# Kernel optimization log

Hardware: AMD Instinct MI355X
Metric: run time of the kernel (lower is better)

The kernel has to match this reference:

```python
import jax, jax.numpy as jnp
import numpy as np

NUM_USERS = 100000
NUM_ITEMS = 50000
N = NUM_USERS + NUM_ITEMS
E = 3000000
DIM = 64


def setup_inputs() -> dict:
    key = jax.random.key(0)
    ks = jax.random.split(key, 8)
    emb_users = 0.01 * jax.random.normal(ks[0], (NUM_USERS, DIM), dtype=jnp.float32)
    emb_items = 0.01 * jax.random.normal(ks[1], (NUM_ITEMS, DIM), dtype=jnp.float32)
    # GCNConv linear weights (bias separate, as in PyG: lin(bias=False) + bias param)
    s = 1.0 / np.sqrt(DIM)
    W1 = jax.random.uniform(ks[2], (DIM, DIM), jnp.float32, -s, s)
    b1 = jnp.zeros((DIM,), jnp.float32)
    W2 = jax.random.uniform(ks[3], (DIM, DIM), jnp.float32, -s, s)
    b2 = jnp.zeros((DIM,), jnp.float32)
    edge_index = jax.random.randint(ks[4], (2, E), 0, N, dtype=jnp.int64)
    edge_weight = jax.random.uniform(ks[5], (E,), jnp.float32)
    return {"emb_users": emb_users, "emb_items": emb_items,
            "W1": W1, "b1": b1, "W2": W2, "b2": b2,
            "edge_index": edge_index, "edge_weight": edge_weight}


def _gcn_conv(x, W, b, row, col):
    """PyG GCNConv with add_self_loops=True, improved=False, unit edge weights.
    out[i] = sum_{j->i} d_j^-1/2 d_i^-1/2 (x_j W) + d_i^-1 (x_i W) + b
    where d includes the self-loop (+1).
    """
    n = x.shape[0]
    xw = x @ W                                           # [N, D]
    deg = jax.ops.segment_sum(jnp.ones_like(row, dtype=x.dtype), col,
                              num_segments=n) + 1.0      # in-degree + self-loop
    dinv = jax.lax.rsqrt(deg)                            # [N]
    coef = dinv[row] * dinv[col]                         # [E]
    msg = xw[row] * coef[:, None]                        # gather + scale  [E, D]
    out = jax.ops.segment_sum(msg, col, num_segments=n)  # scatter-add     [N, D]
    out = out + xw * (dinv * dinv)[:, None]              # self-loop term
    return out + b


def reference(emb_users, emb_items, W1, b1, W2, b2, edge_index, edge_weight):
    # edge_weight is accepted by forward() but never passed to the GCN convs
    row, col = edge_index[0], edge_index[1]
    emb = jnp.concatenate([emb_users, emb_items], axis=0)  # [N, D]
    embs = [emb]
    for W, b in ((W1, b1), (W2, b2)):
        emb = _gcn_conv(emb, W, b, row, col)
        embs.append(emb)
        emb = jax.nn.relu(emb)
    return jnp.stack(embs)  # [num_layers+1, N, D]
```

## Files before the change

kernel.cpp:

```cpp
#include <hip/hip_runtime.h>
#include <hip/hip_fp16.h>

#define DIM 64
#define BPN 1024
#define ECHUNK 8192
#define MAXNB 160

typedef _Float16 f16x8 __attribute__((ext_vector_type(8)));
typedef float f32x4 __attribute__((ext_vector_type(4)));


__global__ __launch_bounds__(1024) void bucket_count_kernel(
    const int* __restrict__ col, int* __restrict__ bucket_cnt, int E, int NB) {
  __shared__ int h[MAXNB];
  for (int t = threadIdx.x; t < NB; t += blockDim.x) h[t] = 0;
  __syncthreads();
  int base = blockIdx.x * ECHUNK;
  int end = min(base + ECHUNK, E);
  for (int e = base + (int)threadIdx.x; e < end; e += blockDim.x)
    atomicAdd(&h[col[e] >> 10], 1);
  __syncthreads();
  for (int t = threadIdx.x; t < NB; t += blockDim.x)
    if (h[t]) atomicAdd(&bucket_cnt[t], h[t]);
}

__global__ void bucket_scan_kernel(const int* __restrict__ bucket_cnt,
                                   int* __restrict__ bucket_base,
                                   int* __restrict__ bucket_cursor,
                                   int* __restrict__ off, int NB, int N, int E) {
  if (threadIdx.x == 0) {
    int s = 0;
    for (int b = 0; b < NB; b++) { bucket_base[b] = s; bucket_cursor[b] = s; s += bucket_cnt[b]; }
    bucket_base[NB] = s;
    off[N] = E;
  }
}

__global__ __launch_bounds__(1024) void bucket_scatter_kernel(
    const int* __restrict__ row, const int* __restrict__ col,
    int* __restrict__ bucket_cursor, int* __restrict__ packed, int E, int NB) {
  __shared__ int h[MAXNB];
  __shared__ int excl0[MAXNB];
  __shared__ int cur[MAXNB];
  __shared__ int gbase[MAXNB];
  __shared__ int staging[ECHUNK];
  __shared__ unsigned short map[ECHUNK];
  const int tid = threadIdx.x;
  for (int t = tid; t < NB; t += blockDim.x) h[t] = 0;
  __syncthreads();
  int base = blockIdx.x * ECHUNK;
  int end = min(base + ECHUNK, E);
  int total = end - base;
  for (int e = base + tid; e < end; e += blockDim.x)
    atomicAdd(&h[col[e] >> 10], 1);
  __syncthreads();
  if (tid == 0) {
    int s = 0;
    for (int b = 0; b < NB; b++) { excl0[b] = s; cur[b] = s; s += h[b]; }
  }
  __syncthreads();
  if (tid < NB) {
    if (h[tid] > 0) gbase[tid] = atomicAdd(&bucket_cursor[tid], h[tid]);
    int s = excl0[tid], c = h[tid];
    for (int j = 0; j < c; j++) map[s + j] = (unsigned short)tid;
  }
  __syncthreads();
  for (int e = base + tid; e < end; e += blockDim.x) {
    int c = col[e];
    int b = c >> 10;
    int pos = atomicAdd(&cur[b], 1);
    staging[pos] = ((c & (BPN - 1)) << 18) | row[e];
  }
  __syncthreads();
  for (int idx = tid; idx < total; idx += blockDim.x) {
    int b = map[idx];
    packed[gbase[b] + idx - excl0[b]] = staging[idx];
  }
}

__global__ __launch_bounds__(1024) void bucket_csr_kernel(
    const int* __restrict__ packed, const int* __restrict__ bucket_base,
    int2* __restrict__ edata, int* __restrict__ off, float* __restrict__ dinv, int N) {
  __shared__ int nh[BPN];
  __shared__ int ncur[BPN];
  __shared__ int wsum[16];
  __shared__ int woff[16];
  const int b = blockIdx.x;
  const int tid = threadIdx.x;
  const int ebase = bucket_base[b];
  const int cnt = bucket_base[b + 1] - ebase;
  nh[tid] = 0;
  __syncthreads();
  for (int i = tid; i < cnt; i += 1024)
    atomicAdd(&nh[packed[ebase + i] >> 18], 1);
  __syncthreads();
  const int lane = tid & 63, wid = tid >> 6;
  int v = nh[tid], x = v;
#pragma unroll
  for (int d = 1; d < 64; d <<= 1) {
    int t = __shfl_up(x, d, 64);
    if (lane >= d) x += t;
  }
  if (lane == 63) wsum[wid] = x;
  __syncthreads();
  if (tid == 0) {
    int s = 0;
#pragma unroll
    for (int k = 0; k < 16; k++) { woff[k] = s; s += wsum[k]; }
  }
  __syncthreads();
  int excl = woff[wid] + x - v;
  ncur[tid] = excl;
  int node = b * BPN + tid;
  if (node < N) {
    off[node] = ebase + excl;
    dinv[node] = rsqrtf((float)v + 1.0f);
  }
  __syncthreads();
  int* edx = (int*)edata;
  for (int i = tid; i < cnt; i += 1024) {
    int p = packed[ebase + i];
    int local = p >> 18;
    int pos = atomicAdd(&ncur[local], 1);
    edx[(size_t)(ebase + pos) * 2] = p & 0x3FFFF;
  }
}

__global__ __launch_bounds__(256) void edge_coef_kernel(
    int2* __restrict__ edata, const float* __restrict__ dinv, int E) {
  int e = blockIdx.x * 256 + threadIdx.x;
  if (e >= E) return;
  int r = ((const int*)edata)[(size_t)e * 2];
  edata[e] = make_int2(r, __float_as_int(dinv[r]));
}

__global__ __launch_bounds__(256) void xw_mfma_kernel(
    const float* __restrict__ xa, const float* __restrict__ xb,
    const float* __restrict__ W, float* __restrict__ out0,
    __half* __restrict__ xwh, int NU, int N, int do_relu) {
  __shared__ _Float16 Wt[64 * 72];
  for (int t = threadIdx.x; t < 4096; t += 256) {
    int k = t >> 6, n = t & 63;
    Wt[n * 72 + k] = (_Float16)W[t];
  }
  __syncthreads();
  const int lane = threadIdx.x & 63;
  const int wid = threadIdx.x >> 6;
  const int m = lane & 15;
  const int quad = lane >> 4;
  f16x8 bfrag[4][2];
#pragma unroll
  for (int c = 0; c < 4; c++)
#pragma unroll
    for (int s = 0; s < 2; s++)
      bfrag[c][s] = *(const f16x8*)&Wt[(c * 16 + m) * 72 + s * 32 + quad * 8];

  const int rbase = (blockIdx.x * 4 + wid) * 16;
  if (rbase >= N) return;
  const int r = rbase + m;
  const int rr = min(r, N - 1);
  const float* src = (xb == nullptr || rr < NU) ? xa + (size_t)rr * DIM
                                                : xb + (size_t)(rr - NU) * DIM;
  f16x8 afrag[2];
#pragma unroll
  for (int s = 0; s < 2; s++) {
    float4 u0 = *(const float4*)(src + s * 32 + quad * 8);
    float4 u1 = *(const float4*)(src + s * 32 + quad * 8 + 4);
    if (out0 != nullptr && r < N) {
      float4* o = (float4*)(out0 + (size_t)r * DIM);
      o[s * 8 + quad * 2] = u0;
      o[s * 8 + quad * 2 + 1] = u1;
    }
    if (do_relu) {
      u0.x = fmaxf(u0.x, 0.f); u0.y = fmaxf(u0.y, 0.f);
      u0.z = fmaxf(u0.z, 0.f); u0.w = fmaxf(u0.w, 0.f);
      u1.x = fmaxf(u1.x, 0.f); u1.y = fmaxf(u1.y, 0.f);
      u1.z = fmaxf(u1.z, 0.f); u1.w = fmaxf(u1.w, 0.f);
    }
    afrag[s][0] = (_Float16)u0.x; afrag[s][1] = (_Float16)u0.y;
    afrag[s][2] = (_Float16)u0.z; afrag[s][3] = (_Float16)u0.w;
    afrag[s][4] = (_Float16)u1.x; afrag[s][5] = (_Float16)u1.y;
    afrag[s][6] = (_Float16)u1.z; afrag[s][7] = (_Float16)u1.w;
  }
  f32x4 acc[4];
#pragma unroll
  for (int c = 0; c < 4; c++) {
    acc[c] = (f32x4){0.f, 0.f, 0.f, 0.f};
    acc[c] = __builtin_amdgcn_mfma_f32_16x16x32_f16(afrag[0], bfrag[c][0], acc[c], 0, 0, 0);
    acc[c] = __builtin_amdgcn_mfma_f32_16x16x32_f16(afrag[1], bfrag[c][1], acc[c], 0, 0, 0);
  }
#pragma unroll
  for (int reg = 0; reg < 4; reg++) {
    int orow = rbase + quad * 4 + reg;
    if (orow < N) {
      __half* dst = xwh + (size_t)orow * DIM + m;
#pragma unroll
      for (int c = 0; c < 4; c++)
        dst[c * 16] = __float2half(acc[c][reg]);
    }
  }
}

__global__ void aggregate_kernel(const __half* __restrict__ xwh, const int* __restrict__ off,
                                 const int2* __restrict__ edata, const float* __restrict__ dinv,
                                 const float* __restrict__ b, float* __restrict__ out, int n) {
  const int lane = threadIdx.x & 63;
  const int i = blockIdx.x * (blockDim.x >> 6) + (threadIdx.x >> 6);
  if (i >= n) return;
  const int esel = lane >> 3;
  const int j = lane & 7;
  const float di = dinv[i];
  float acc[8];
#pragma unroll
  for (int q = 0; q < 8; q++) acc[q] = 0.0f;
  if (esel == 0) {
    float4 f = ((const float4*)xwh)[(size_t)i * 8 + j];
    const __half2* h = (const __half2*)&f;
#pragma unroll
    for (int q = 0; q < 4; q++) {
      float2 p = __half22float2(h[q]);
      acc[2 * q] = di * p.x;
      acc[2 * q + 1] = di * p.y;
    }
  }
  int s0 = off[i], s1 = off[i + 1];
  for (int s = s0; s < s1; s += 64) {
    int m = s1 - s;
    if (m > 64) m = 64;
    int myr = 0;
    float myc = 0.0f;
    if (lane < m) {
      int2 v = edata[s + lane];
      myr = v.x;
      myc = __int_as_float(v.y);
    }
    int r0 = __shfl(myr, esel, 64);
    float c0 = __shfl(myc, esel, 64);
    float4 f0 = ((const float4*)xwh)[(size_t)r0 * 8 + j];
    for (int k = 8; k < m; k += 8) {
      int r1 = __shfl(myr, k + esel, 64);
      float c1 = __shfl(myc, k + esel, 64);
      float4 f1 = ((const float4*)xwh)[(size_t)r1 * 8 + j];
      const __half2* h0 = (const __half2*)&f0;
#pragma unroll
      for (int q = 0; q < 4; q++) {
        float2 p = __half22float2(h0[q]);
        acc[2 * q] += c0 * p.x;
        acc[2 * q + 1] += c0 * p.y;
      }
      f0 = f1;
      c0 = c1;
    }
    const __half2* h0 = (const __half2*)&f0;
#pragma unroll
    for (int q = 0; q < 4; q++) {
      float2 p = __half22float2(h0[q]);
      acc[2 * q] += c0 * p.x;
      acc[2 * q + 1] += c0 * p.y;
    }
  }
#pragma unroll
  for (int q = 0; q < 8; q++) {
    acc[q] += __shfl_xor(acc[q], 8, 64);
    acc[q] += __shfl_xor(acc[q], 16, 64);
    acc[q] += __shfl_xor(acc[q], 32, 64);
  }
  if (esel == 0) {
    float4 b0 = ((const float4*)b)[2 * j];
    float4 b1 = ((const float4*)b)[2 * j + 1];
    float4* orow = (float4*)(out + (size_t)i * DIM);
    orow[2 * j] = make_float4(di * acc[0] + b0.x, di * acc[1] + b0.y,
                              di * acc[2] + b0.z, di * acc[3] + b0.w);
    orow[2 * j + 1] = make_float4(di * acc[4] + b1.x, di * acc[5] + b1.y,
                                  di * acc[6] + b1.z, di * acc[7] + b1.w);
  }
}

extern "C" void kernel_launch(void* const* d_in, const int* in_sizes, int n_in,
                              void* d_out, int out_size, void* d_ws, size_t ws_size,
                              hipStream_t stream) {
  const float* emb_users = (const float*)d_in[0];
  const float* emb_items = (const float*)d_in[1];
  const float* W1 = (const float*)d_in[2];
  const float* b1 = (const float*)d_in[3];
  const float* W2 = (const float*)d_in[4];
  const float* b2 = (const float*)d_in[5];
  const int* edge_index = (const int*)d_in[6];

  const int NU = in_sizes[0] / DIM;
  const int NI = in_sizes[1] / DIM;
  const int N = NU + NI;
  const int E = in_sizes[6] / 2;
  const int NB = (N + BPN - 1) / BPN;
  const int* row = edge_index;
  const int* col = edge_index + E;

  float* out = (float*)d_out;

  char* ws = (char*)d_ws;
  size_t o = 0;
  auto alloc = [&](size_t bytes) -> void* {
    o = (o + 255) & ~(size_t)255;
    void* p = ws + o;
    o += bytes;
    return p;
  };
  int* bucket_cnt    = (int*)alloc((size_t)NB * 4);
  int* bucket_base   = (int*)alloc((size_t)(NB + 1) * 4);
  int* bucket_cursor = (int*)alloc((size_t)NB * 4);
  int* off           = (int*)alloc((size_t)(N + 1) * 4);
  float* dinv        = (float*)alloc((size_t)N * 4);
  int2* edata        = (int2*)alloc((size_t)E * 8);
  __half* xwh        = (__half*)alloc((size_t)N * DIM * 2);
  int* packed        = (int*)xwh;
  (void)ws_size;

  const int nbE = (E + ECHUNK - 1) / ECHUNK;

  hipMemsetAsync(bucket_cnt, 0, (size_t)NB * 4, stream);
  bucket_count_kernel<<<nbE, 1024, 0, stream>>>(col, bucket_cnt, E, NB);
  bucket_scan_kernel<<<1, 64, 0, stream>>>(bucket_cnt, bucket_base, bucket_cursor, off, NB, N, E);
  bucket_scatter_kernel<<<nbE, 1024, 0, stream>>>(row, col, bucket_cursor, packed, E, NB);
  bucket_csr_kernel<<<NB, 1024, 0, stream>>>(packed, bucket_base, edata, off, dinv, N);
  edge_coef_kernel<<<(E + 255) / 256, 256, 0, stream>>>(edata, dinv, E);

  const int TB = 256;
  const int gr = (N + 3) / 4;
  const int gx = (N + 63) / 64;

  xw_mfma_kernel<<<gx, TB, 0, stream>>>(emb_users, emb_items, W1, out, xwh, NU, N, 0);
  aggregate_kernel<<<gr, TB, 0, stream>>>((const __half*)xwh, off, edata, dinv, b1,
                                          out + (size_t)N * DIM, N);

  xw_mfma_kernel<<<gx, TB, 0, stream>>>(out + (size_t)N * DIM, nullptr, W2, nullptr, xwh, N, N, 1);
  aggregate_kernel<<<gr, TB, 0, stream>>>((const __half*)xwh, off, edata, dinv, b2,
                                          out + (size_t)2 * N * DIM, N);
}
```

Baseline: 425.3 us.

## Unroll aggregation gather four edges per lane and store CSR rows densely

The aggregation loop no longer loads 64 edges into lanes and broadcasts them with shuffles. Each 8-lane group now reads its own edge records directly and issues four independent row gathers per iteration, which raises memory-level parallelism. Out-of-range slots are clamped to the last edge and given a zero coefficient. Separately, the CSR build writes row indices to a dense int buffer instead of a strided int2 slot. This avoids half-empty scattered writes, at the cost of an extra E-sized buffer and a separate read in the coefficient kernel.

```diff
diff --git a/kernel.cpp b/kernel.cpp
--- a/kernel.cpp
+++ b/kernel.cpp
@@ -80,7 +80,7 @@
 
 __global__ __launch_bounds__(1024) void bucket_csr_kernel(
     const int* __restrict__ packed, const int* __restrict__ bucket_base,
-    int2* __restrict__ edata, int* __restrict__ off, float* __restrict__ dinv, int N) {
+    int* __restrict__ perm_row, int* __restrict__ off, float* __restrict__ dinv, int N) {
   __shared__ int nh[BPN];
   __shared__ int ncur[BPN];
   __shared__ int wsum[16];
@@ -117,20 +117,20 @@
     dinv[node] = rsqrtf((float)v + 1.0f);
   }
   __syncthreads();
-  int* edx = (int*)edata;
   for (int i = tid; i < cnt; i += 1024) {
     int p = packed[ebase + i];
     int local = p >> 18;
     int pos = atomicAdd(&ncur[local], 1);
-    edx[(size_t)(ebase + pos) * 2] = p & 0x3FFFF;
+    perm_row[ebase + pos] = p & 0x3FFFF;
   }
 }
 
 __global__ __launch_bounds__(256) void edge_coef_kernel(
-    int2* __restrict__ edata, const float* __restrict__ dinv, int E) {
+    const int* __restrict__ perm_row, const float* __restrict__ dinv,
+    int2* __restrict__ edata, int E) {
   int e = blockIdx.x * 256 + threadIdx.x;
   if (e >= E) return;
-  int r = ((const int*)edata)[(size_t)e * 2];
+  int r = perm_row[e];
   edata[e] = make_int2(r, __float_as_int(dinv[r]));
 }
 
@@ -210,11 +210,12 @@
   const int esel = lane >> 3;
   const int j = lane & 7;
   const float di = dinv[i];
+  const float4* rows = (const float4*)xwh;
   float acc[8];
 #pragma unroll
   for (int q = 0; q < 8; q++) acc[q] = 0.0f;
   if (esel == 0) {
-    float4 f = ((const float4*)xwh)[(size_t)i * 8 + j];
+    float4 f = rows[(size_t)i * 8 + j];
     const __half2* h = (const __half2*)&f;
 #pragma unroll
     for (int q = 0; q < 4; q++) {
@@ -223,40 +224,49 @@
       acc[2 * q + 1] = di * p.y;
     }
   }
-  int s0 = off[i], s1 = off[i + 1];
-  for (int s = s0; s < s1; s += 64) {
-    int m = s1 - s;
-    if (m > 64) m = 64;
-    int myr = 0;
-    float myc = 0.0f;
-    if (lane < m) {
-      int2 v = edata[s + lane];
-      myr = v.x;
-      myc = __int_as_float(v.y);
-    }
-    int r0 = __shfl(myr, esel, 64);
-    float c0 = __shfl(myc, esel, 64);
-    float4 f0 = ((const float4*)xwh)[(size_t)r0 * 8 + j];
-    for (int k = 8; k < m; k += 8) {
-      int r1 = __shfl(myr, k + esel, 64);
-      float c1 = __shfl(myc, k + esel, 64);
-      float4 f1 = ((const float4*)xwh)[(size_t)r1 * 8 + j];
-      const __half2* h0 = (const __half2*)&f0;
-#pragma unroll
-      for (int q = 0; q < 4; q++) {
-        float2 p = __half22float2(h0[q]);
-        acc[2 * q] += c0 * p.x;
-        acc[2 * q + 1] += c0 * p.y;
-      }
-      f0 = f1;
-      c0 = c1;
-    }
+  const int s0 = off[i], s1 = off[i + 1];
+  const int last = s1 - 1;
+  for (int k = s0; k < s1; k += 32) {
+    const int e0 = k + esel, e1 = e0 + 8, e2 = e0 + 16, e3 = e0 + 24;
+    int2 v0 = edata[min(e0, last)];
+    int2 v1 = edata[min(e1, last)];
+    int2 v2 = edata[min(e2, last)];
+    int2 v3 = edata[min(e3, last)];
+    float c0 = (e0 <= last) ? __int_as_float(v0.y) : 0.0f;
+    float c1 = (e1 <= last) ? __int_as_float(v1.y) : 0.0f;
+    float c2 = (e2 <= last) ? __int_as_float(v2.y) : 0.0f;
+    float c3 = (e3 <= last) ? __int_as_float(v3.y) : 0.0f;
+    float4 f0 = rows[(size_t)v0.x * 8 + j];
+    float4 f1 = rows[(size_t)v1.x * 8 + j];
+    float4 f2 = rows[(size_t)v2.x * 8 + j];
+    float4 f3 = rows[(size_t)v3.x * 8 + j];
     const __half2* h0 = (const __half2*)&f0;
-#pragma unroll
-    for (int q = 0; q < 4; q++) {
-      float2 p = __half22float2(h0[q]);
-      acc[2 * q] += c0 * p.x;
-      acc[2 * q + 1] += c0 * p.y;
+    const __half2* h1 = (const __half2*)&f1;
+    const __half2* h2 = (const __half2*)&f2;
+    const __half2* h3 = (const __half2*)&f3;
+#pragma unroll
+    for (int q = 0; q < 4; q++) {
+      float2 p0 = __half22float2(h0[q]);
+      acc[2 * q] += c0 * p0.x;
+      acc[2 * q + 1] += c0 * p0.y;
+    }
+#pragma unroll
+    for (int q = 0; q < 4; q++) {
+      float2 p1 = __half22float2(h1[q]);
+      acc[2 * q] += c1 * p1.x;
+      acc[2 * q + 1] += c1 * p1.y;
+    }
+#pragma unroll
+    for (int q = 0; q < 4; q++) {
+      float2 p2 = __half22float2(h2[q]);
+      acc[2 * q] += c2 * p2.x;
+      acc[2 * q + 1] += c2 * p2.y;
+    }
+#pragma unroll
+    for (int q = 0; q < 4; q++) {
+      float2 p3 = __half22float2(h3[q]);
+      acc[2 * q] += c3 * p3.x;
+      acc[2 * q + 1] += c3 * p3.y;
     }
   }
 #pragma unroll
@@ -310,6 +320,7 @@
   int* bucket_cursor = (int*)alloc((size_t)NB * 4);
   int* off           = (int*)alloc((size_t)(N + 1) * 4);
   float* dinv        = (float*)alloc((size_t)N * 4);
+  int* perm_row      = (int*)alloc((size_t)E * 4);
   int2* edata        = (int2*)alloc((size_t)E * 8);
   __half* xwh        = (__half*)alloc((size_t)N * DIM * 2);
   int* packed        = (int*)xwh;
@@ -321,8 +332,8 @@
   bucket_count_kernel<<<nbE, 1024, 0, stream>>>(col, bucket_cnt, E, NB);
   bucket_scan_kernel<<<1, 64, 0, stream>>>(bucket_cnt, bucket_base, bucket_cursor, off, NB, N, E);
   bucket_scatter_kernel<<<nbE, 1024, 0, stream>>>(row, col, bucket_cursor, packed, E, NB);
-  bucket_csr_kernel<<<NB, 1024, 0, stream>>>(packed, bucket_base, edata, off, dinv, N);
-  edge_coef_kernel<<<(E + 255) / 256, 256, 0, stream>>>(edata, dinv, E);
+  bucket_csr_kernel<<<NB, 1024, 0, stream>>>(packed, bucket_base, perm_row, off, dinv, N);
+  edge_coef_kernel<<<(E + 255) / 256, 256, 0, stream>>>(perm_row, dinv, edata, E);
 
   const int TB = 256;
   const int gr = (N + 3) / 4;
```

Result: faster. 405.5 us (-4.6%).
